# Performance work log

Measured on AMD Instinct MI355X. Metric: run time of the kernel, lower is better.

## Reference

```python
import jax, jax.numpy as jnp
import numpy as np
from jax import lax

_SHARPEN = jnp.array([[-1., -1., -1.], [-1., 9., -1.], [-1., -1., -1.]], dtype=jnp.float32)


def setup_inputs() -> dict:
    key = jax.random.key(0)
    k1, k2, k3, k4, k5 = jax.random.split(key, 5)
    B, C, H, W = 32, 3, 512, 512
    x = jax.random.uniform(k1, (B, C, H, W), dtype=jnp.float32)
    gamma = 0.5 + jax.random.uniform(k2, (B,), dtype=jnp.float32)            # [0.5, 1.5)
    wb = 0.8 + 0.4 * jax.random.uniform(k3, (B, 3), dtype=jnp.float32)       # [0.8, 1.2)
    contrast = 0.8 + 0.4 * jax.random.uniform(k4, (B,), dtype=jnp.float32)   # [0.8, 1.2)
    sharpen_strength = jax.random.uniform(k5, (B,), dtype=jnp.float32)       # [0, 1)
    return {"x": x, "gamma": gamma, "wb": wb, "contrast": contrast,
            "sharpen_strength": sharpen_strength}


def reference(x, gamma, wb, contrast, sharpen_strength):
    B, C, H, W = x.shape
    g = gamma[:, None, None, None]
    x = x ** g                                       # tone curve
    x = x * wb[:, :, None, None]                     # white balance
    mean = jnp.mean(x, axis=(2, 3), keepdims=True)   # per-channel mean
    x = jnp.clip((x - mean) * contrast[:, None, None, None] + mean, 0.0, 1.0)
    # depthwise 3x3 sharpen (same kernel per channel)
    kern = jnp.tile(_SHARPEN.astype(x.dtype)[None, None], (C, 1, 1, 1))  # [C,1,3,3]
    x_sharp = lax.conv_general_dilated(
        x, kern, window_strides=(1, 1), padding=((1, 1), (1, 1)),
        dimension_numbers=("NCHW", "OIHW", "NCHW"), feature_group_count=C)
    s = sharpen_strength[:, None, None, None]
    return jnp.clip(x_sharp * s + x * (1.0 - s), 0.0, 1.0)
```

## Files before the change

kernel.cpp:

```cpp
#include <hip/hip_runtime.h>


#define HH 512
#define WW 512
#define NPLANE (HH * WW)
#define NPLANES 96
#define CHUNKS 8

__device__ __forceinline__ float fpow(float v, float g) {
    return __builtin_amdgcn_exp2f(g * __builtin_amdgcn_logf(v));
}

__device__ __forceinline__ float tfm(float v, float g, float wbc, float mean, float ct) {
    float p = fpow(v, g) * wbc;
    float t = (p - mean) * ct + mean;
    return __saturatef(t);
}

__global__ __launch_bounds__(256) void mean_kernel(
    const float* __restrict__ x,
    const float* __restrict__ gamma,
    const float* __restrict__ wb,
    float* __restrict__ sums)
{
    const int blk   = blockIdx.x;
    const int plane = blk / CHUNKS;
    const int chunk = blk % CHUNKS;
    const int b     = plane / 3;
    const float g   = gamma[b];
    const float wbc = wb[plane];

    const float4* xp = (const float4*)(x + (size_t)plane * NPLANE)
                       + (size_t)chunk * (NPLANE / CHUNKS / 4);
    const int tid = threadIdx.x;

    float acc = 0.f;
    #pragma unroll
    for (int i = 0; i < 32; ++i) {
        float4 v = xp[i * 256 + tid];
        acc += fpow(v.x, g) + fpow(v.y, g) + fpow(v.z, g) + fpow(v.w, g);
    }

    #pragma unroll
    for (int off = 32; off > 0; off >>= 1)
        acc += __shfl_down(acc, off, 64);

    __shared__ float wsum[4];
    const int wave = tid >> 6;
    const int lane = tid & 63;
    if (lane == 0) wsum[wave] = acc;
    __syncthreads();
    if (tid == 0) {
        float s = (wsum[0] + wsum[1] + wsum[2] + wsum[3]) * wbc;
        atomicAdd(&sums[plane], s);
    }
}

#define TR 16
#define LSTRIDE 520

__global__ __launch_bounds__(256) void fuse_kernel(
    const float* __restrict__ x,
    const float* __restrict__ gamma,
    const float* __restrict__ wb,
    const float* __restrict__ contrast,
    const float* __restrict__ sharpen,
    const float* __restrict__ sums,
    float* __restrict__ out)
{
    __shared__ float tile[(TR + 2) * LSTRIDE];

    const int plane = blockIdx.y;
    const int tileY = blockIdx.x;
    const int b     = plane / 3;
    const float g    = gamma[b];
    const float wbc  = wb[plane];
    const float ct   = contrast[b];
    const float s    = sharpen[b];
    const float mean = sums[plane] * (1.0f / (float)NPLANE);

    const float* xp = x + (size_t)plane * NPLANE;
    const int y0  = tileY * TR;
    const int tid = threadIdx.x;

    #pragma unroll
    for (int ii = 0; ii < 9; ++ii) {
        int i  = ii * 256 + tid;
        int r  = i >> 7;
        int c4 = i & 127;
        int gy = y0 - 1 + r;
        float4* dst = (float4*)&tile[r * LSTRIDE + 4 + c4 * 4];
        if (gy < 0 || gy >= HH) {
            *dst = make_float4(0.f, 0.f, 0.f, 0.f);
        } else {
            float4 v = ((const float4*)(xp + (size_t)gy * WW))[c4];
            *dst = make_float4(tfm(v.x, g, wbc, mean, ct),
                               tfm(v.y, g, wbc, mean, ct),
                               tfm(v.z, g, wbc, mean, ct),
                               tfm(v.w, g, wbc, mean, ct));
        }
    }
    if (tid < TR + 2) {
        tile[tid * LSTRIDE + 3]   = 0.f;
        tile[tid * LSTRIDE + 516] = 0.f;
    }
    __syncthreads();

    float* op = out + (size_t)plane * NPLANE;
    const float c1 = 1.0f + 9.0f * s;

    const int lane = tid & 63;
    const int wave = tid >> 6;

    #pragma unroll
    for (int ii = 0; ii < 8; ++ii) {
        int t   = ii * 4 + wave;
        int rg  = t & 3;
        int cg  = t >> 2;
        int c   = cg * 64 + lane;
        int oy0 = rg * 4;

        float h[6], mid[4];
        #pragma unroll
        for (int j = 0; j < 6; ++j) {
            const float* rp = &tile[(oy0 + j) * LSTRIDE + 4 + c];
            float a = rp[-1], m = rp[0], d = rp[1];
            h[j] = a + m + d;
            if (j >= 1 && j <= 4) mid[j - 1] = m;
        }
        #pragma unroll
        for (int j = 0; j < 4; ++j) {
            float o = __saturatef(c1 * mid[j] - s * (h[j] + h[j + 1] + h[j + 2]));
            op[(size_t)(y0 + oy0 + j) * WW + c] = o;
        }
    }
}

extern "C" void kernel_launch(void* const* d_in, const int* in_sizes, int n_in,
                              void* d_out, int out_size, void* d_ws, size_t ws_size,
                              hipStream_t stream) {
    const float* x        = (const float*)d_in[0];
    const float* gamma    = (const float*)d_in[1];
    const float* wb       = (const float*)d_in[2];
    const float* contrast = (const float*)d_in[3];
    const float* sharpen  = (const float*)d_in[4];
    float* out  = (float*)d_out;
    float* sums = (float*)d_ws;

    hipMemsetAsync(sums, 0, NPLANES * sizeof(float), stream);
    mean_kernel<<<dim3(NPLANES * CHUNKS), 256, 0, stream>>>(x, gamma, wb, sums);
    fuse_kernel<<<dim3(32, NPLANES), 256, 0, stream>>>(x, gamma, wb, contrast,
                                                       sharpen, sums, out);
}
```

Before: 209.9 us.

## Replace atomic mean with per-chunk partials and vectorize sharpen stencil with streaming stores

The mean kernel now writes one partial sum per block instead of atomically adding into a zeroed buffer, so the memset launch and the atomics go away. The fuse kernel sums the eight partials itself and applies the white-balance factor there. The sharpen stage is restructured so each thread handles four adjacent columns across eight rows. It reuses horizontal sums in a sliding window, reads LDS with 128-bit loads, and writes float4 results with nontemporal stores. An occupancy hint of four blocks per CU is added, which may limit registers.

```diff
diff --git a/kernel.cpp b/kernel.cpp
--- a/kernel.cpp
+++ b/kernel.cpp
@@ -7,31 +7,27 @@
 #define NPLANES 96
 #define CHUNKS 8
 
+typedef float f4 __attribute__((ext_vector_type(4)));
+
 __device__ __forceinline__ float fpow(float v, float g) {
     return __builtin_amdgcn_exp2f(g * __builtin_amdgcn_logf(v));
 }
-
 __device__ __forceinline__ float tfm(float v, float g, float wbc, float mean, float ct) {
     float p = fpow(v, g) * wbc;
-    float t = (p - mean) * ct + mean;
-    return __saturatef(t);
+    return __saturatef((p - mean) * ct + mean);
 }
 
 __global__ __launch_bounds__(256) void mean_kernel(
     const float* __restrict__ x,
     const float* __restrict__ gamma,
-    const float* __restrict__ wb,
-    float* __restrict__ sums)
+    float* __restrict__ partials)
 {
     const int blk   = blockIdx.x;
     const int plane = blk / CHUNKS;
-    const int chunk = blk % CHUNKS;
-    const int b     = plane / 3;
-    const float g   = gamma[b];
-    const float wbc = wb[plane];
+    const float g   = gamma[plane / 3];
 
     const float4* xp = (const float4*)(x + (size_t)plane * NPLANE)
-                       + (size_t)chunk * (NPLANE / CHUNKS / 4);
+                       + (size_t)(blk % CHUNKS) * (NPLANE / CHUNKS / 4);
     const int tid = threadIdx.x;
 
     float acc = 0.f;
@@ -40,32 +36,26 @@
         float4 v = xp[i * 256 + tid];
         acc += fpow(v.x, g) + fpow(v.y, g) + fpow(v.z, g) + fpow(v.w, g);
     }
-
     #pragma unroll
     for (int off = 32; off > 0; off >>= 1)
         acc += __shfl_down(acc, off, 64);
 
     __shared__ float wsum[4];
-    const int wave = tid >> 6;
-    const int lane = tid & 63;
-    if (lane == 0) wsum[wave] = acc;
+    if ((tid & 63) == 0) wsum[tid >> 6] = acc;
     __syncthreads();
-    if (tid == 0) {
-        float s = (wsum[0] + wsum[1] + wsum[2] + wsum[3]) * wbc;
-        atomicAdd(&sums[plane], s);
-    }
+    if (tid == 0) partials[blk] = wsum[0] + wsum[1] + wsum[2] + wsum[3];
 }
 
 #define TR 16
 #define LSTRIDE 520
 
-__global__ __launch_bounds__(256) void fuse_kernel(
+__global__ __launch_bounds__(256, 4) void fuse_kernel(
     const float* __restrict__ x,
     const float* __restrict__ gamma,
     const float* __restrict__ wb,
     const float* __restrict__ contrast,
     const float* __restrict__ sharpen,
-    const float* __restrict__ sums,
+    const float* __restrict__ partials,
     float* __restrict__ out)
 {
     __shared__ float tile[(TR + 2) * LSTRIDE];
@@ -73,11 +63,16 @@
     const int plane = blockIdx.y;
     const int tileY = blockIdx.x;
     const int b     = plane / 3;
-    const float g    = gamma[b];
-    const float wbc  = wb[plane];
-    const float ct   = contrast[b];
-    const float s    = sharpen[b];
-    const float mean = sums[plane] * (1.0f / (float)NPLANE);
+    const float g   = gamma[b];
+    const float wbc = wb[plane];
+    const float ct  = contrast[b];
+    const float s   = sharpen[b];
+
+    float psum = 0.f;
+    const float* pp = partials + plane * CHUNKS;
+    #pragma unroll
+    for (int i = 0; i < CHUNKS; ++i) psum += pp[i];
+    const float mean = psum * wbc * (1.0f / (float)NPLANE);
 
     const float* xp = x + (size_t)plane * NPLANE;
     const int y0  = tileY * TR;
@@ -111,28 +106,38 @@
 
     const int lane = tid & 63;
     const int wave = tid >> 6;
+    const int cg   = wave & 1;
+    const int rg   = wave >> 1;
+    const int c0   = cg * 256 + lane * 4;
+    const int jb   = rg * 8;
 
-    #pragma unroll
-    for (int ii = 0; ii < 8; ++ii) {
-        int t   = ii * 4 + wave;
-        int rg  = t & 3;
-        int cg  = t >> 2;
-        int c   = cg * 64 + lane;
-        int oy0 = rg * 4;
+    auto ldrow = [&](int r, f4& h, f4& m) {
+        const float* p = &tile[r * LSTRIDE + c0];
+        f4 A = *(const f4*)(p);
+        f4 B = *(const f4*)(p + 4);
+        f4 C = *(const f4*)(p + 8);
+        h.x = A.w + B.x + B.y;
+        h.y = B.x + B.y + B.z;
+        h.z = B.y + B.z + B.w;
+        h.w = B.z + B.w + C.x;
+        m = B;
+    };
 
-        float h[6], mid[4];
-        #pragma unroll
-        for (int j = 0; j < 6; ++j) {
-            const float* rp = &tile[(oy0 + j) * LSTRIDE + 4 + c];
-            float a = rp[-1], m = rp[0], d = rp[1];
-            h[j] = a + m + d;
-            if (j >= 1 && j <= 4) mid[j - 1] = m;
-        }
-        #pragma unroll
-        for (int j = 0; j < 4; ++j) {
-            float o = __saturatef(c1 * mid[j] - s * (h[j] + h[j + 1] + h[j + 2]));
-            op[(size_t)(y0 + oy0 + j) * WW + c] = o;
-        }
+    f4 h0, h1, h2, m1, m2, mdum;
+    ldrow(jb,     h0, mdum);
+    ldrow(jb + 1, h1, m1);
+
+    #pragma unroll 4
+    for (int j = 0; j < 8; ++j) {
+        ldrow(jb + 2 + j, h2, m2);
+        f4 sum = h0 + h1 + h2;
+        f4 o;
+        o.x = __saturatef(fmaf(c1, m1.x, -s * sum.x));
+        o.y = __saturatef(fmaf(c1, m1.y, -s * sum.y));
+        o.z = __saturatef(fmaf(c1, m1.z, -s * sum.z));
+        o.w = __saturatef(fmaf(c1, m1.w, -s * sum.w));
+        __builtin_nontemporal_store(o, (f4*)(op + (size_t)(y0 + jb + j) * WW + c0));
+        h0 = h1; h1 = h2; m1 = m2;
     }
 }
 
@@ -144,11 +149,10 @@
     const float* wb       = (const float*)d_in[2];
     const float* contrast = (const float*)d_in[3];
     const float* sharpen  = (const float*)d_in[4];
-    float* out  = (float*)d_out;
-    float* sums = (float*)d_ws;
+    float* out      = (float*)d_out;
+    float* partials = (float*)d_ws;
 
-    hipMemsetAsync(sums, 0, NPLANES * sizeof(float), stream);
-    mean_kernel<<<dim3(NPLANES * CHUNKS), 256, 0, stream>>>(x, gamma, wb, sums);
+    mean_kernel<<<dim3(NPLANES * CHUNKS), 256, 0, stream>>>(x, gamma, partials);
     fuse_kernel<<<dim3(32, NPLANES), 256, 0, stream>>>(x, gamma, wb, contrast,
-                                                       sharpen, sums, out);
+                                                       sharpen, partials, out);
 }
```

Measured after the change: 199.2 us. -5.1%, faster.
